# Kernel tuning notes

Measured on AMD Instinct MI355X. Metric: run time of the kernel, lower is better.

The kernel has to match this reference:

```python
import jax, jax.numpy as jnp
from jax import lax
import numpy as np

GAMMA = 1.0
N, M = 4096, 4096


def setup_inputs() -> dict:
    key = jax.random.key(0)
    D = jax.random.normal(key, (N, M), dtype=jnp.float32)
    return {"D": D}


def reference(D):
    # Faithful translation of the original forward.
    # Step 1: the module overwrites D with exp(-D/gamma); the DP then runs on E.
    E = jnp.exp(-D / GAMMA)  # [N, M]

    # Step 2: hard-min DP (torch.min, despite the "Soft" name):
    #   c[i,j] = E[i,j] + min(c[i-1,j], c[i,j-1], c[i-1,j-1])
    # Row-wise vectorization: within row i, with a[j] = min(prev[j], prev[j-1])
    # (a[0] = prev[0]), the within-row recursion c[j] = E[j] + min(a[j], c[j-1])
    # unrolls to   c[j] = S[j] + cummin(a - S_shift)[j],  S = cumsum(E_row).
    row0 = jnp.cumsum(E[0])  # first row: pure left-to-right accumulation

    def step(prev, e_row):
        a = jnp.minimum(prev, jnp.concatenate([prev[:1], prev[:-1]]))
        S = jnp.cumsum(e_row)
        Sm1 = jnp.concatenate([jnp.zeros((1,), e_row.dtype), S[:-1]])
        c = S + lax.cummin(a - Sm1)
        return c, None

    last_row, _ = lax.scan(step, row0, E[1:])
    cost = last_row[-1]  # acc_cost[N-1, M-1]

    # Step 3: acc_grad. In the original row-major loop, acc_grad[i,j] is still 0
    # when cell (i,j) is processed (all writers come later), so each cell
    # simply (a) subtracts d[i,j]/gamma from itself and (b) adds d[i,j]/gamma to
    # its (i-1,j-1), (i-1,j), (i,j-1) neighbors, with d = exp(-E/gamma).
    # Fully vectorizable as a shifted stencil:
    d = jnp.exp(-E / GAMMA)
    dp = jnp.pad(d, ((0, 1), (0, 1)))  # zero-pad bottom/right for boundary cells
    acc_grad = (dp[1:, 1:] + dp[1:, :-1] + dp[:-1, 1:] - d) / GAMMA

    return cost, acc_grad
```

## Files before the change

kernel.cpp:

```cpp
#include <hip/hip_runtime.h>
#include <math.h>

#define NN 4096
#define STRIPS 32
#define SW 128
#define RING_ROWS 256
#define RINGB (RING_ROWS * SW * 4)
#define BATCH 64
#define NBATCH 65
#define PAD 64
#define COLPITCH (NN + 2 * PAD)
#define INFV 1e30f
#define SENTU 0xFFFFFFFFu

__device__ __forceinline__ float dpp_wave_shr1(float x) {
    return __int_as_float(__builtin_amdgcn_update_dpp(
        0, __float_as_int(x), 0x138 , 0xf, 0xf, false));
}

__device__ __forceinline__ float bload(const unsigned* colL, int row) {
    const int rowc = (row < NN) ? row : (NN - 1);
    unsigned u = __hip_atomic_load(colL + rowc, __ATOMIC_RELAXED,
                                   __HIP_MEMORY_SCOPE_AGENT);
    return __uint_as_float(u);
}

__device__ __forceinline__ bool has_sent(float b, int rb, int lane) {
    return __any(((rb + lane) < NN) && (__float_as_uint(b) == SENTU));
}

__device__ __forceinline__ void stageB(const float* Sg, float* ring, int rb,
                                       int lane) {
    #pragma unroll
    for (int k = 0; k < 32; ++k) {
        const int r0 = rb + 2 * k;
        const int r0c = (r0 < NN - 1) ? r0 : (NN - 2);
        const int slot = r0 & (RING_ROWS - 1);
        const float* gsrc =
            Sg + (size_t)(r0c + (lane >> 5)) * NN + ((lane & 31) << 2);
        __builtin_amdgcn_global_load_lds(
            (const __attribute__((address_space(1))) unsigned*)gsrc,
            (__attribute__((address_space(3))) unsigned*)((char*)ring +
                                                         slot * (SW * 4)),
            16, 0, 0);
    }
}

template <int DOEXP>
__global__ __launch_bounds__(128, 1) void dtw_dp(const float* __restrict__ S,
                                                 float* __restrict__ cost_out,
                                                 unsigned* __restrict__ colbuf) {
    __shared__ float ring[RING_ROWS * SW];
    __shared__ float inbox[2][BATCH];
    __shared__ float outbox[BATCH];
    __shared__ float outdummy[64];

    const int tid = threadIdx.x;
    const int lane = tid & 63;
    const int b = blockIdx.x;
    const int g = ((b & 7) << 2) | (b >> 3);

    const float* Sg = S + g * SW;
    const unsigned* colL = colbuf + (size_t)(g - 1) * COLPITCH + PAD;
    unsigned* colM = colbuf + (size_t)g * COLPITCH + PAD;

    if (tid < 64) {
        {
            const float4 z = make_float4(0.f, 0.f, 0.f, 0.f);
            float4* r4 = reinterpret_cast<float4*>(&ring[192 * SW]);
            #pragma unroll
            for (int i = 0; i < 32; ++i) r4[i * 64 + lane] = z;
        }
        asm volatile("s_waitcnt lgkmcnt(0)" ::: "memory");
        __builtin_amdgcn_s_barrier();

        const bool lane0 = (lane == 0);
        const int ostep = (lane == 63) ? 1 : 0;
        float cur0 = INFV, cur1 = INFV;
        float l1s = INFV, l2s = INFV;
        float bprevc = INFV;
        float save = 0.f;

        unsigned caddr = ((unsigned)((0 - lane) & (RING_ROWS - 1)) << 9) |
                         ((unsigned)lane << 3);

        for (int n = 0; n < NBATCH; ++n) {
            const int tb = n << 6;
            const float binb = inbox[n & 1][lane];

            float2 rv[BATCH];
            #pragma unroll
            for (int s = 0; s < BATCH; ++s)
                rv[s] = *reinterpret_cast<const float2*>(
                    (const char*)ring +
                    ((caddr + (unsigned)(s * 512)) & (RINGB - 1)));

            float* obp = (lane == 63) ? &outbox[0] : &outdummy[lane];
            float pbc = INFV;
            #pragma unroll
            for (int s = 0; s < BATCH; ++s) {
                float e0, e1;
                if (DOEXP) { e0 = __expf(-rv[s].x); e1 = __expf(-rv[s].y); }
                else       { e0 = rv[s].x;          e1 = rv[s].y; }
                float bcur;
                if (g == 0)
                    bcur = (n == 0 && s == 0) ? 0.f : INFV;
                else
                    bcur = __int_as_float(
                        __builtin_amdgcn_readlane(__float_as_int(binb), s));
                const float bpv =
                    (g == 0) ? INFV : ((s == 0) ? bprevc : pbc);
                const float L1 = lane0 ? bcur : l1s;
                const float L2 = lane0 ? bpv : l2s;
                const float m0 = fminf(fminf(L1, cur0), L2);
                const float c0 = e0 + m0;
                const float c1 = e1 + fminf(c0, fminf(cur0, cur1));
                *obp = c1;
                obp += ostep;
                const float sh = dpp_wave_shr1(c1);
                l2s = l1s; l1s = sh;
                cur0 = c0; cur1 = c1;
                pbc = bcur;
                if (s == 62) save = c1;
            }
            bprevc = pbc;
            caddr = (caddr + (unsigned)(BATCH * 512)) & (RINGB - 1);

            asm volatile("s_waitcnt lgkmcnt(0)" ::: "memory");
            {
                const float ob = outbox[lane];
                asm volatile("s_waitcnt lgkmcnt(0)" ::: "memory");
                __hip_atomic_store(colM + (tb - 63 + lane),
                                   __float_as_uint(ob), __ATOMIC_RELAXED,
                                   __HIP_MEMORY_SCOPE_AGENT);
            }
            __builtin_amdgcn_s_barrier();
        }

        if (g == STRIPS - 1 && lane == 63) cost_out[0] = save;
    } else {
        stageB(Sg, ring, 0, lane);
        stageB(Sg, ring, 64, lane);
        float qv = INFV;
        if (g > 0) {
            qv = bload(colL, lane);
            while (has_sent(qv, 0, lane)) qv = bload(colL, lane);
            inbox[0][lane] = qv;
            qv = bload(colL, 64 + lane);
        }
        asm volatile("s_waitcnt vmcnt(0) lgkmcnt(0)" ::: "memory");
        __builtin_amdgcn_s_barrier();

        for (int n = 0; n < NBATCH; ++n) {
            const int tb = n << 6;
            if (g > 0) {
                const int vb = tb + 64;
                while (has_sent(qv, vb, lane)) qv = bload(colL, vb + lane);
                inbox[(n + 1) & 1][lane] = qv;
                qv = bload(colL, tb + 128 + lane);
            }
            stageB(Sg, ring, tb + 128, lane);
            __builtin_amdgcn_sched_barrier(0);
            if (g > 0) asm volatile("s_waitcnt vmcnt(33)" ::: "memory");
            else       asm volatile("s_waitcnt vmcnt(32)" ::: "memory");
            __builtin_amdgcn_sched_barrier(0);
            asm volatile("s_waitcnt lgkmcnt(0)" ::: "memory");
            __builtin_amdgcn_s_barrier();
        }
    }
}

__global__ __launch_bounds__(256) void eg_kernel(const float* __restrict__ D,
                                                 float* __restrict__ E,
                                                 float* __restrict__ G) {
    const int idx = blockIdx.x * 256 + threadIdx.x;
    const int i = idx >> 10;
    const int j = (idx & 1023) << 2;
    if (i >= NN) return;

    const float* row0 = D + (size_t)i * NN + j;
    const bool hasR = (i + 1) < NN;
    const bool hasC = (j + 4) < NN;

    const float4 r0 = *reinterpret_cast<const float4*>(row0);
    float4 r1 = make_float4(0.f, 0.f, 0.f, 0.f);
    if (hasR) r1 = *reinterpret_cast<const float4*>(row0 + NN);
    const float s0 = hasC ? row0[4] : 0.f;
    const float s1 = (hasR && hasC) ? row0[NN + 4] : 0.f;

    const float ex0 = __expf(-r0.x), ex1 = __expf(-r0.y);
    const float ex2 = __expf(-r0.z), ex3 = __expf(-r0.w);
    *reinterpret_cast<float4*>(E + (size_t)i * NN + j) =
        make_float4(ex0, ex1, ex2, ex3);

    const float a0 = __expf(-ex0), a1 = __expf(-ex1);
    const float a2 = __expf(-ex2), a3 = __expf(-ex3);
    const float a4 = hasC ? __expf(-__expf(-s0)) : 0.f;
    const float b0 = hasR ? __expf(-__expf(-r1.x)) : 0.f;
    const float b1 = hasR ? __expf(-__expf(-r1.y)) : 0.f;
    const float b2 = hasR ? __expf(-__expf(-r1.z)) : 0.f;
    const float b3 = hasR ? __expf(-__expf(-r1.w)) : 0.f;
    const float b4 = (hasR && hasC) ? __expf(-__expf(-s1)) : 0.f;

    float* go = G + (size_t)i * NN + j;
    go[0] = b1 + b0 + a1 - a0;
    go[1] = b2 + b1 + a2 - a1;
    go[2] = b3 + b2 + a3 - a2;
    go[3] = b4 + b3 + a4 - a3;
}

__device__ __forceinline__ float dfun(float x) { return __expf(-__expf(-x)); }

__global__ __launch_bounds__(256) void dtw_grad_kernel(const float* __restrict__ D,
                                                       float* __restrict__ G) {
    const int idx = blockIdx.x * 256 + threadIdx.x;
    const int i = idx >> 10;
    const int j = (idx & 1023) << 2;
    if (i >= NN) return;

    const float* row0 = D + (size_t)i * NN + j;
    const bool hasR = (i + 1) < NN;
    const bool hasC = (j + 4) < NN;

    const float4 r0 = *reinterpret_cast<const float4*>(row0);
    float4 r1 = make_float4(0.f, 0.f, 0.f, 0.f);
    if (hasR) r1 = *reinterpret_cast<const float4*>(row0 + NN);
    const float s0 = hasC ? row0[4] : 0.f;
    const float s1 = (hasR && hasC) ? row0[NN + 4] : 0.f;

    const float a0 = dfun(r0.x), a1 = dfun(r0.y), a2 = dfun(r0.z), a3 = dfun(r0.w);
    const float a4 = hasC ? dfun(s0) : 0.f;
    const float b0 = hasR ? dfun(r1.x) : 0.f;
    const float b1 = hasR ? dfun(r1.y) : 0.f;
    const float b2 = hasR ? dfun(r1.z) : 0.f;
    const float b3 = hasR ? dfun(r1.w) : 0.f;
    const float b4 = (hasR && hasC) ? dfun(s1) : 0.f;

    float* go = G + (size_t)i * NN + j;
    go[0] = b1 + b0 + a1 - a0;
    go[1] = b2 + b1 + a2 - a1;
    go[2] = b3 + b2 + a3 - a2;
    go[3] = b4 + b3 + a4 - a3;
}

extern "C" void kernel_launch(void* const* d_in, const int* in_sizes, int n_in,
                              void* d_out, int out_size, void* d_ws, size_t ws_size,
                              hipStream_t stream) {
    (void)in_sizes; (void)n_in; (void)out_size;
    const float* D = (const float*)d_in[0];
    float* out = (float*)d_out;

    const size_t colbytes = (size_t)STRIPS * COLPITCH * sizeof(unsigned);
    const size_t ebytes = (size_t)NN * NN * sizeof(float);
    const int gblocks = (NN * (NN / 4)) / 256;

    if (ws_size >= ebytes + colbytes) {
        float* E = (float*)d_ws;
        unsigned* colbuf = (unsigned*)((char*)d_ws + ebytes);
        hipMemsetAsync(colbuf, 0xFF, colbytes, stream);
        eg_kernel<<<gblocks, 256, 0, stream>>>(D, E, out + 1);
        dtw_dp<0><<<STRIPS, 128, 0, stream>>>(E, out, colbuf);
    } else {
        unsigned* colbuf = (ws_size >= colbytes) ? (unsigned*)d_ws
                                                 : (unsigned*)(out + 1);
        hipMemsetAsync(colbuf, 0xFF, colbytes, stream);
        dtw_dp<1><<<STRIPS, 128, 0, stream>>>(D, out, colbuf);
        dtw_grad_kernel<<<gblocks, 256, 0, stream>>>(D, out + 1);
    }
}
```

Baseline: 491.6 us.

## Merge producer/consumer waves into single-wave DP and fuse exp into DP

Removes the separate staging wave and its per-batch barriers. The compute wave now issues its own async global-to-LDS loads, polls the neighbour-strip column and computes exp(-D) inline. It also drops the precompute pass that wrote E to the workspace, so the DP reads D directly and the gradient kernel runs afterward. This saves a full NxN write and read plus the barrier handoff. The cost is exp on the serial critical path, and load latency that is now hidden only by vmcnt pipelining inside one wave.

```diff
diff --git a/kernel.cpp b/kernel.cpp
--- a/kernel.cpp
+++ b/kernel.cpp
@@ -46,167 +46,109 @@
     }
 }
 
-template <int DOEXP>
-__global__ __launch_bounds__(128, 1) void dtw_dp(const float* __restrict__ S,
-                                                 float* __restrict__ cost_out,
-                                                 unsigned* __restrict__ colbuf) {
+__global__ __launch_bounds__(64, 1) void dtw_dp(const float* __restrict__ D,
+                                                float* __restrict__ cost_out,
+                                                unsigned* __restrict__ colbuf) {
     __shared__ float ring[RING_ROWS * SW];
-    __shared__ float inbox[2][BATCH];
     __shared__ float outbox[BATCH];
     __shared__ float outdummy[64];
 
-    const int tid = threadIdx.x;
-    const int lane = tid & 63;
+    const int lane = threadIdx.x;
     const int b = blockIdx.x;
     const int g = ((b & 7) << 2) | (b >> 3);
 
-    const float* Sg = S + g * SW;
+    const float* Dg = D + g * SW;
     const unsigned* colL = colbuf + (size_t)(g - 1) * COLPITCH + PAD;
     unsigned* colM = colbuf + (size_t)g * COLPITCH + PAD;
-
-    if (tid < 64) {
+    const bool lane0 = (lane == 0);
+    const int ostep = (lane == 63) ? 1 : 0;
+
+    {
+        const float4 z = make_float4(0.f, 0.f, 0.f, 0.f);
+        float4* r4 = reinterpret_cast<float4*>(&ring[192 * SW]);
+        #pragma unroll
+        for (int i = 0; i < 32; ++i) r4[i * 64 + lane] = z;
+    }
+
+    stageB(Dg, ring, 0, lane);
+    stageB(Dg, ring, 64, lane);
+    float qv = INFV;
+    if (g > 0) qv = bload(colL, lane);
+    asm volatile("s_waitcnt vmcnt(0) lgkmcnt(0)" ::: "memory");
+
+    float cur0 = INFV, cur1 = INFV;
+    float l1s = INFV, l2s = INFV;
+    float bprevc = INFV;
+    float save = 0.f;
+
+    unsigned caddr = ((unsigned)((0 - lane) & (RING_ROWS - 1)) << 9) |
+                     ((unsigned)lane << 3);
+
+    for (int n = 0; n < NBATCH; ++n) {
+        const int tb = n << 6;
+
+        if (g > 0) {
+            while (has_sent(qv, tb, lane)) qv = bload(colL, tb + lane);
+        }
+
+        __builtin_amdgcn_sched_barrier(0);
+        if (g > 0) asm volatile("s_waitcnt vmcnt(34)" ::: "memory");
+        else       asm volatile("s_waitcnt vmcnt(33)" ::: "memory");
+        __builtin_amdgcn_sched_barrier(0);
+
+        float qvn = INFV;
+        if (g > 0) qvn = bload(colL, tb + 64 + lane);
+
+        float2 rv[BATCH];
+        #pragma unroll
+        for (int s = 0; s < BATCH; ++s)
+            rv[s] = *reinterpret_cast<const float2*>(
+                (const char*)ring +
+                ((caddr + (unsigned)(s * 512)) & (RINGB - 1)));
+
+        float* obp = (lane == 63) ? &outbox[0] : &outdummy[lane];
+        float pbc = INFV;
+        #pragma unroll
+        for (int s = 0; s < BATCH; ++s) {
+            const float e0 = __expf(-rv[s].x);
+            const float e1 = __expf(-rv[s].y);
+            float bcur;
+            if (g == 0)
+                bcur = (n == 0 && s == 0) ? 0.f : INFV;
+            else
+                bcur = __int_as_float(
+                    __builtin_amdgcn_readlane(__float_as_int(qv), s));
+            const float bpv = (g == 0) ? INFV : ((s == 0) ? bprevc : pbc);
+            const float L1 = lane0 ? bcur : l1s;
+            const float L2 = lane0 ? bpv : l2s;
+            const float m0 = fminf(fminf(L1, cur0), L2);
+            const float c0 = e0 + m0;
+            const float c1 = e1 + fminf(c0, fminf(cur0, cur1));
+            *obp = c1;
+            obp += ostep;
+            const float sh = dpp_wave_shr1(c1);
+            l2s = l1s; l1s = sh;
+            cur0 = c0; cur1 = c1;
+            pbc = bcur;
+            if (s == 62) save = c1;
+        }
+        bprevc = pbc;
+        caddr = (caddr + (unsigned)(BATCH * 512)) & (RINGB - 1);
+
+        asm volatile("s_waitcnt lgkmcnt(0)" ::: "memory");
         {
-            const float4 z = make_float4(0.f, 0.f, 0.f, 0.f);
-            float4* r4 = reinterpret_cast<float4*>(&ring[192 * SW]);
-            #pragma unroll
-            for (int i = 0; i < 32; ++i) r4[i * 64 + lane] = z;
+            const float ob = outbox[lane];
+            asm volatile("s_waitcnt lgkmcnt(0)" ::: "memory");
+            __hip_atomic_store(colM + (tb - 63 + lane), __float_as_uint(ob),
+                               __ATOMIC_RELAXED, __HIP_MEMORY_SCOPE_AGENT);
         }
-        asm volatile("s_waitcnt lgkmcnt(0)" ::: "memory");
-        __builtin_amdgcn_s_barrier();
-
-        const bool lane0 = (lane == 0);
-        const int ostep = (lane == 63) ? 1 : 0;
-        float cur0 = INFV, cur1 = INFV;
-        float l1s = INFV, l2s = INFV;
-        float bprevc = INFV;
-        float save = 0.f;
-
-        unsigned caddr = ((unsigned)((0 - lane) & (RING_ROWS - 1)) << 9) |
-                         ((unsigned)lane << 3);
-
-        for (int n = 0; n < NBATCH; ++n) {
-            const int tb = n << 6;
-            const float binb = inbox[n & 1][lane];
-
-            float2 rv[BATCH];
-            #pragma unroll
-            for (int s = 0; s < BATCH; ++s)
-                rv[s] = *reinterpret_cast<const float2*>(
-                    (const char*)ring +
-                    ((caddr + (unsigned)(s * 512)) & (RINGB - 1)));
-
-            float* obp = (lane == 63) ? &outbox[0] : &outdummy[lane];
-            float pbc = INFV;
-            #pragma unroll
-            for (int s = 0; s < BATCH; ++s) {
-                float e0, e1;
-                if (DOEXP) { e0 = __expf(-rv[s].x); e1 = __expf(-rv[s].y); }
-                else       { e0 = rv[s].x;          e1 = rv[s].y; }
-                float bcur;
-                if (g == 0)
-                    bcur = (n == 0 && s == 0) ? 0.f : INFV;
-                else
-                    bcur = __int_as_float(
-                        __builtin_amdgcn_readlane(__float_as_int(binb), s));
-                const float bpv =
-                    (g == 0) ? INFV : ((s == 0) ? bprevc : pbc);
-                const float L1 = lane0 ? bcur : l1s;
-                const float L2 = lane0 ? bpv : l2s;
-                const float m0 = fminf(fminf(L1, cur0), L2);
-                const float c0 = e0 + m0;
-                const float c1 = e1 + fminf(c0, fminf(cur0, cur1));
-                *obp = c1;
-                obp += ostep;
-                const float sh = dpp_wave_shr1(c1);
-                l2s = l1s; l1s = sh;
-                cur0 = c0; cur1 = c1;
-                pbc = bcur;
-                if (s == 62) save = c1;
-            }
-            bprevc = pbc;
-            caddr = (caddr + (unsigned)(BATCH * 512)) & (RINGB - 1);
-
-            asm volatile("s_waitcnt lgkmcnt(0)" ::: "memory");
-            {
-                const float ob = outbox[lane];
-                asm volatile("s_waitcnt lgkmcnt(0)" ::: "memory");
-                __hip_atomic_store(colM + (tb - 63 + lane),
-                                   __float_as_uint(ob), __ATOMIC_RELAXED,
-                                   __HIP_MEMORY_SCOPE_AGENT);
-            }
-            __builtin_amdgcn_s_barrier();
-        }
-
-        if (g == STRIPS - 1 && lane == 63) cost_out[0] = save;
-    } else {
-        stageB(Sg, ring, 0, lane);
-        stageB(Sg, ring, 64, lane);
-        float qv = INFV;
-        if (g > 0) {
-            qv = bload(colL, lane);
-            while (has_sent(qv, 0, lane)) qv = bload(colL, lane);
-            inbox[0][lane] = qv;
-            qv = bload(colL, 64 + lane);
-        }
-        asm volatile("s_waitcnt vmcnt(0) lgkmcnt(0)" ::: "memory");
-        __builtin_amdgcn_s_barrier();
-
-        for (int n = 0; n < NBATCH; ++n) {
-            const int tb = n << 6;
-            if (g > 0) {
-                const int vb = tb + 64;
-                while (has_sent(qv, vb, lane)) qv = bload(colL, vb + lane);
-                inbox[(n + 1) & 1][lane] = qv;
-                qv = bload(colL, tb + 128 + lane);
-            }
-            stageB(Sg, ring, tb + 128, lane);
-            __builtin_amdgcn_sched_barrier(0);
-            if (g > 0) asm volatile("s_waitcnt vmcnt(33)" ::: "memory");
-            else       asm volatile("s_waitcnt vmcnt(32)" ::: "memory");
-            __builtin_amdgcn_sched_barrier(0);
-            asm volatile("s_waitcnt lgkmcnt(0)" ::: "memory");
-            __builtin_amdgcn_s_barrier();
-        }
+
+        stageB(Dg, ring, tb + 128, lane);
+
+        qv = qvn;
     }
-}
-
-__global__ __launch_bounds__(256) void eg_kernel(const float* __restrict__ D,
-                                                 float* __restrict__ E,
-                                                 float* __restrict__ G) {
-    const int idx = blockIdx.x * 256 + threadIdx.x;
-    const int i = idx >> 10;
-    const int j = (idx & 1023) << 2;
-    if (i >= NN) return;
-
-    const float* row0 = D + (size_t)i * NN + j;
-    const bool hasR = (i + 1) < NN;
-    const bool hasC = (j + 4) < NN;
-
-    const float4 r0 = *reinterpret_cast<const float4*>(row0);
-    float4 r1 = make_float4(0.f, 0.f, 0.f, 0.f);
-    if (hasR) r1 = *reinterpret_cast<const float4*>(row0 + NN);
-    const float s0 = hasC ? row0[4] : 0.f;
-    const float s1 = (hasR && hasC) ? row0[NN + 4] : 0.f;
-
-    const float ex0 = __expf(-r0.x), ex1 = __expf(-r0.y);
-    const float ex2 = __expf(-r0.z), ex3 = __expf(-r0.w);
-    *reinterpret_cast<float4*>(E + (size_t)i * NN + j) =
-        make_float4(ex0, ex1, ex2, ex3);
-
-    const float a0 = __expf(-ex0), a1 = __expf(-ex1);
-    const float a2 = __expf(-ex2), a3 = __expf(-ex3);
-    const float a4 = hasC ? __expf(-__expf(-s0)) : 0.f;
-    const float b0 = hasR ? __expf(-__expf(-r1.x)) : 0.f;
-    const float b1 = hasR ? __expf(-__expf(-r1.y)) : 0.f;
-    const float b2 = hasR ? __expf(-__expf(-r1.z)) : 0.f;
-    const float b3 = hasR ? __expf(-__expf(-r1.w)) : 0.f;
-    const float b4 = (hasR && hasC) ? __expf(-__expf(-s1)) : 0.f;
-
-    float* go = G + (size_t)i * NN + j;
-    go[0] = b1 + b0 + a1 - a0;
-    go[1] = b2 + b1 + a2 - a1;
-    go[2] = b3 + b2 + a3 - a2;
-    go[3] = b4 + b3 + a4 - a3;
+
+    if (g == STRIPS - 1 && lane == 63) cost_out[0] = save;
 }
 
 __device__ __forceinline__ float dfun(float x) { return __expf(-__expf(-x)); }
@@ -251,20 +193,12 @@
     float* out = (float*)d_out;
 
     const size_t colbytes = (size_t)STRIPS * COLPITCH * sizeof(unsigned);
-    const size_t ebytes = (size_t)NN * NN * sizeof(float);
     const int gblocks = (NN * (NN / 4)) / 256;
 
-    if (ws_size >= ebytes + colbytes) {
-        float* E = (float*)d_ws;
-        unsigned* colbuf = (unsigned*)((char*)d_ws + ebytes);
-        hipMemsetAsync(colbuf, 0xFF, colbytes, stream);
-        eg_kernel<<<gblocks, 256, 0, stream>>>(D, E, out + 1);
-        dtw_dp<0><<<STRIPS, 128, 0, stream>>>(E, out, colbuf);
-    } else {
-        unsigned* colbuf = (ws_size >= colbytes) ? (unsigned*)d_ws
-                                                 : (unsigned*)(out + 1);
-        hipMemsetAsync(colbuf, 0xFF, colbytes, stream);
-        dtw_dp<1><<<STRIPS, 128, 0, stream>>>(D, out, colbuf);
-        dtw_grad_kernel<<<gblocks, 256, 0, stream>>>(D, out + 1);
-    }
-}
+    unsigned* colbuf = (ws_size >= colbytes) ? (unsigned*)d_ws
+                                             : (unsigned*)(out + 1);
+
+    hipMemsetAsync(colbuf, 0xFF, colbytes, stream);
+    dtw_dp<<<STRIPS, 64, 0, stream>>>(D, out, colbuf);
+    dtw_grad_kernel<<<gblocks, 256, 0, stream>>>(D, out + 1);
+}
```

After: 602.6 us. +22.6%, slower.

## Replace producer/consumer LDS ring with single-wave register double-buffered DP

Applied to the files above, without the earlier changes.

The DP kernel drops the separate loader wave, the LDS ring buffer and the per-batch barriers. A single wave now loads the next 32 anti-diagonal rows of E straight from global memory into registers while it computes the current batch. It publishes boundary values directly from lane 63 with atomic stores instead of going through an LDS outbox. This removes barrier and LDS round-trip latency from the serial critical path, but global load latency must now be hidden by register double-buffering, and the smaller batch means more polling steps.

```diff
diff --git a/kernel.cpp b/kernel.cpp
--- a/kernel.cpp
+++ b/kernel.cpp
@@ -4,10 +4,7 @@
 #define NN 4096
 #define STRIPS 32
 #define SW 128
-#define RING_ROWS 256
-#define RINGB (RING_ROWS * SW * 4)
-#define BATCH 64
-#define NBATCH 65
+#define BATCH 32
 #define PAD 64
 #define COLPITCH (NN + 2 * PAD)
 #define INFV 1e30f
@@ -18,156 +15,118 @@
         0, __float_as_int(x), 0x138 , 0xf, 0xf, false));
 }
 
-__device__ __forceinline__ float bload(const unsigned* colL, int row) {
+__device__ __forceinline__ float bload(const unsigned* colL, int row, int lane) {
+    float v = INFV;
     const int rowc = (row < NN) ? row : (NN - 1);
-    unsigned u = __hip_atomic_load(colL + rowc, __ATOMIC_RELAXED,
-                                   __HIP_MEMORY_SCOPE_AGENT);
-    return __uint_as_float(u);
+    if (lane < 32) {
+        unsigned u = __hip_atomic_load(colL + rowc, __ATOMIC_RELAXED,
+                                       __HIP_MEMORY_SCOPE_AGENT);
+        v = __uint_as_float(u);
+    }
+    return v;
 }
 
 __device__ __forceinline__ bool has_sent(float b, int rb, int lane) {
-    return __any(((rb + lane) < NN) && (__float_as_uint(b) == SENTU));
-}
-
-__device__ __forceinline__ void stageB(const float* Sg, float* ring, int rb,
-                                       int lane) {
-    #pragma unroll
-    for (int k = 0; k < 32; ++k) {
-        const int r0 = rb + 2 * k;
-        const int r0c = (r0 < NN - 1) ? r0 : (NN - 2);
-        const int slot = r0 & (RING_ROWS - 1);
-        const float* gsrc =
-            Sg + (size_t)(r0c + (lane >> 5)) * NN + ((lane & 31) << 2);
-        __builtin_amdgcn_global_load_lds(
-            (const __attribute__((address_space(1))) unsigned*)gsrc,
-            (__attribute__((address_space(3))) unsigned*)((char*)ring +
-                                                         slot * (SW * 4)),
-            16, 0, 0);
-    }
-}
+    return __any((lane < 32) && ((rb + lane) < NN) &&
+                 (__float_as_uint(b) == SENTU));
+}
+
+#define ELOAD(BUF, RB, CLAMP) do {                                          \
+    _Pragma("unroll")                                                       \
+    for (int s_ = 0; s_ < BATCH; ++s_) {                                    \
+        int row_ = (RB) + s_ - lane;                                        \
+        if (CLAMP) row_ = (row_ < 0) ? 0 : ((row_ > NN - 1) ? NN - 1 : row_);\
+        BUF[s_] = *reinterpret_cast<const float2*>(                         \
+            Sg + (size_t)row_ * NN + (lane << 1));                          \
+    }                                                                       \
+} while (0)
+
+#define CSTEP(CUR, NXT, N, CLAMP) do {                                      \
+    const int n_ = (N);                                                     \
+    const int tb_ = n_ * BATCH;                                             \
+    if (comm) {                                                             \
+        while (has_sent(qv, tb_, lane))                                     \
+            qv = bload(colL, tb_ + (lane & 31), lane);                      \
+    }                                                                       \
+    float qvn = INFV;                                                       \
+    if (comm) qvn = bload(colL, tb_ + BATCH + (lane & 31), lane);           \
+    __builtin_amdgcn_sched_barrier(0);                                      \
+    ELOAD(NXT, tb_ + BATCH, CLAMP);                                         \
+    __builtin_amdgcn_sched_barrier(0);                                      \
+    float pbc = INFV;                                                       \
+    _Pragma("unroll")                                                       \
+    for (int s_ = 0; s_ < BATCH; ++s_) {                                    \
+        float e0, e1;                                                       \
+        if (DOEXP) { e0 = __expf(-CUR[s_].x); e1 = __expf(-CUR[s_].y); }    \
+        else       { e0 = CUR[s_].x;          e1 = CUR[s_].y; }             \
+        if (CLAMP && (tb_ + s_ - lane) < 0) { e0 = 0.f; e1 = 0.f; }         \
+        float bcur;                                                         \
+        if (g == 0)                                                         \
+            bcur = (n_ == 0 && s_ == 0) ? 0.f : INFV;     \
+        else                                                                \
+            bcur = __int_as_float(                                          \
+                __builtin_amdgcn_readlane(__float_as_int(qv), s_));         \
+        const float bpv = (g == 0) ? INFV : ((s_ == 0) ? bprevc : pbc);     \
+        const float L1 = lane0 ? bcur : l1s;             \
+        const float L2 = lane0 ? bpv : l2s;              \
+        const float m0 = fminf(fminf(L1, cur0), L2);                        \
+        const float c0 = e0 + m0;                                           \
+        const float c1 = e1 + fminf(c0, fminf(cur0, cur1));                 \
+        csave[s_] = c1;                                                     \
+        const float sh = dpp_wave_shr1(c1);                                 \
+        l2s = l1s; l1s = sh;                                                \
+        cur0 = c0; cur1 = c1;                                               \
+        pbc = bcur;                                                         \
+        if (n_ == 129 && s_ == 30) save = c1;        \
+    }                                                                       \
+    bprevc = pbc;                                                           \
+    if (lane == 63) {                                                       \
+        _Pragma("unroll")                                                   \
+        for (int s_ = 0; s_ < BATCH; ++s_)                                  \
+            __hip_atomic_store(colM + (tb_ - 63 + s_),                      \
+                               __float_as_uint(csave[s_]),                  \
+                               __ATOMIC_RELAXED, __HIP_MEMORY_SCOPE_AGENT); \
+    }                                                                       \
+    qv = qvn;                                                               \
+} while (0)
 
 template <int DOEXP>
-__global__ __launch_bounds__(128, 1) void dtw_dp(const float* __restrict__ S,
-                                                 float* __restrict__ cost_out,
-                                                 unsigned* __restrict__ colbuf) {
-    __shared__ float ring[RING_ROWS * SW];
-    __shared__ float inbox[2][BATCH];
-    __shared__ float outbox[BATCH];
-    __shared__ float outdummy[64];
-
-    const int tid = threadIdx.x;
-    const int lane = tid & 63;
+__global__ __launch_bounds__(64) void dtw_dp(const float* __restrict__ S,
+                                             float* __restrict__ cost_out,
+                                             unsigned* __restrict__ colbuf) {
+    const int lane = threadIdx.x;
     const int b = blockIdx.x;
     const int g = ((b & 7) << 2) | (b >> 3);
 
     const float* Sg = S + g * SW;
     const unsigned* colL = colbuf + (size_t)(g - 1) * COLPITCH + PAD;
     unsigned* colM = colbuf + (size_t)g * COLPITCH + PAD;
-
-    if (tid < 64) {
-        {
-            const float4 z = make_float4(0.f, 0.f, 0.f, 0.f);
-            float4* r4 = reinterpret_cast<float4*>(&ring[192 * SW]);
-            #pragma unroll
-            for (int i = 0; i < 32; ++i) r4[i * 64 + lane] = z;
-        }
-        asm volatile("s_waitcnt lgkmcnt(0)" ::: "memory");
-        __builtin_amdgcn_s_barrier();
-
-        const bool lane0 = (lane == 0);
-        const int ostep = (lane == 63) ? 1 : 0;
-        float cur0 = INFV, cur1 = INFV;
-        float l1s = INFV, l2s = INFV;
-        float bprevc = INFV;
-        float save = 0.f;
-
-        unsigned caddr = ((unsigned)((0 - lane) & (RING_ROWS - 1)) << 9) |
-                         ((unsigned)lane << 3);
-
-        for (int n = 0; n < NBATCH; ++n) {
-            const int tb = n << 6;
-            const float binb = inbox[n & 1][lane];
-
-            float2 rv[BATCH];
-            #pragma unroll
-            for (int s = 0; s < BATCH; ++s)
-                rv[s] = *reinterpret_cast<const float2*>(
-                    (const char*)ring +
-                    ((caddr + (unsigned)(s * 512)) & (RINGB - 1)));
-
-            float* obp = (lane == 63) ? &outbox[0] : &outdummy[lane];
-            float pbc = INFV;
-            #pragma unroll
-            for (int s = 0; s < BATCH; ++s) {
-                float e0, e1;
-                if (DOEXP) { e0 = __expf(-rv[s].x); e1 = __expf(-rv[s].y); }
-                else       { e0 = rv[s].x;          e1 = rv[s].y; }
-                float bcur;
-                if (g == 0)
-                    bcur = (n == 0 && s == 0) ? 0.f : INFV;
-                else
-                    bcur = __int_as_float(
-                        __builtin_amdgcn_readlane(__float_as_int(binb), s));
-                const float bpv =
-                    (g == 0) ? INFV : ((s == 0) ? bprevc : pbc);
-                const float L1 = lane0 ? bcur : l1s;
-                const float L2 = lane0 ? bpv : l2s;
-                const float m0 = fminf(fminf(L1, cur0), L2);
-                const float c0 = e0 + m0;
-                const float c1 = e1 + fminf(c0, fminf(cur0, cur1));
-                *obp = c1;
-                obp += ostep;
-                const float sh = dpp_wave_shr1(c1);
-                l2s = l1s; l1s = sh;
-                cur0 = c0; cur1 = c1;
-                pbc = bcur;
-                if (s == 62) save = c1;
-            }
-            bprevc = pbc;
-            caddr = (caddr + (unsigned)(BATCH * 512)) & (RINGB - 1);
-
-            asm volatile("s_waitcnt lgkmcnt(0)" ::: "memory");
-            {
-                const float ob = outbox[lane];
-                asm volatile("s_waitcnt lgkmcnt(0)" ::: "memory");
-                __hip_atomic_store(colM + (tb - 63 + lane),
-                                   __float_as_uint(ob), __ATOMIC_RELAXED,
-                                   __HIP_MEMORY_SCOPE_AGENT);
-            }
-            __builtin_amdgcn_s_barrier();
-        }
-
-        if (g == STRIPS - 1 && lane == 63) cost_out[0] = save;
-    } else {
-        stageB(Sg, ring, 0, lane);
-        stageB(Sg, ring, 64, lane);
-        float qv = INFV;
-        if (g > 0) {
-            qv = bload(colL, lane);
-            while (has_sent(qv, 0, lane)) qv = bload(colL, lane);
-            inbox[0][lane] = qv;
-            qv = bload(colL, 64 + lane);
-        }
-        asm volatile("s_waitcnt vmcnt(0) lgkmcnt(0)" ::: "memory");
-        __builtin_amdgcn_s_barrier();
-
-        for (int n = 0; n < NBATCH; ++n) {
-            const int tb = n << 6;
-            if (g > 0) {
-                const int vb = tb + 64;
-                while (has_sent(qv, vb, lane)) qv = bload(colL, vb + lane);
-                inbox[(n + 1) & 1][lane] = qv;
-                qv = bload(colL, tb + 128 + lane);
-            }
-            stageB(Sg, ring, tb + 128, lane);
-            __builtin_amdgcn_sched_barrier(0);
-            if (g > 0) asm volatile("s_waitcnt vmcnt(33)" ::: "memory");
-            else       asm volatile("s_waitcnt vmcnt(32)" ::: "memory");
-            __builtin_amdgcn_sched_barrier(0);
-            asm volatile("s_waitcnt lgkmcnt(0)" ::: "memory");
-            __builtin_amdgcn_s_barrier();
-        }
+    const bool comm = (g > 0);
+    const bool lane0 = (lane == 0);
+
+    float cur0 = INFV, cur1 = INFV;
+    float l1s = INFV, l2s = INFV;
+    float bprevc = INFV;
+    float save = 0.f;
+    float csave[BATCH];
+    float2 eC[BATCH], eN[BATCH];
+
+    float qv = INFV;
+    if (comm) qv = bload(colL, lane & 31, lane);
+    ELOAD(eC, 0, true);
+
+    CSTEP(eC, eN, 0, true);
+    CSTEP(eN, eC, 1, true);
+    for (int i = 1; i <= 62; ++i) {
+        CSTEP(eC, eN, 2 * i, false);
+        CSTEP(eN, eC, 2 * i + 1, false);
     }
+    CSTEP(eC, eN, 126, true);
+    CSTEP(eN, eC, 127, true);
+    CSTEP(eC, eN, 128, true);
+    CSTEP(eN, eC, 129, true);
+
+    if (g == STRIPS - 1 && lane == 63) cost_out[0] = save;
 }
 
 __global__ __launch_bounds__(256) void eg_kernel(const float* __restrict__ D,
@@ -257,14 +216,14 @@
     if (ws_size >= ebytes + colbytes) {
         float* E = (float*)d_ws;
         unsigned* colbuf = (unsigned*)((char*)d_ws + ebytes);
-        hipMemsetAsync(colbuf, 0xFF, colbytes, stream);
+        (void)hipMemsetAsync(colbuf, 0xFF, colbytes, stream);
         eg_kernel<<<gblocks, 256, 0, stream>>>(D, E, out + 1);
-        dtw_dp<0><<<STRIPS, 128, 0, stream>>>(E, out, colbuf);
+        dtw_dp<0><<<STRIPS, 64, 0, stream>>>(E, out, colbuf);
     } else {
         unsigned* colbuf = (ws_size >= colbytes) ? (unsigned*)d_ws
                                                  : (unsigned*)(out + 1);
-        hipMemsetAsync(colbuf, 0xFF, colbytes, stream);
-        dtw_dp<1><<<STRIPS, 128, 0, stream>>>(D, out, colbuf);
+        (void)hipMemsetAsync(colbuf, 0xFF, colbytes, stream);
+        dtw_dp<1><<<STRIPS, 64, 0, stream>>>(D, out, colbuf);
         dtw_grad_kernel<<<gblocks, 256, 0, stream>>>(D, out + 1);
     }
 }
```

New measurement: 731.0 us. +48.7%, slower.
